# Optimization experiments

Hardware: AMD Instinct MI355X
Metric: run time of the kernel (lower is better)

## Reference

```python
import jax, jax.numpy as jnp
from jax import lax
import numpy as np

PATCH_H = 8
PATCH_W = 8


def setup_inputs() -> dict:
    key = jax.random.key(0)
    k1, k2 = jax.random.split(key)
    x = jax.random.normal(k1, (2, 1024, 256, 256), dtype=jnp.float32)
    # Conv1d weight [C_out, C_in, k], bias=False
    conv_w = jax.random.normal(k2, (1024, 1024, 3), dtype=jnp.float32) * 0.02
    return {"x": x, "conv_w": conv_w}


def reference(x, conv_w):
    B, C, H, W = x.shape
    hf, wf = H // PATCH_H, W // PATCH_W
    P = hf * wf
    # Patch average pool: mean over each (PATCH_H, PATCH_W) tile -> [B, C, hf, wf]
    xp = x.reshape(B, C, hf, PATCH_H, wf, PATCH_W)
    y = xp.mean(axis=(3, 5)).reshape(B, C, P)
    # Conv1d over the patch axis (SAME padding, no bias), then sigmoid gate
    g = lax.conv_general_dilated(
        y, conv_w, window_strides=(1,), padding="SAME",
        dimension_numbers=("NCH", "OIH", "NCH"))
    g = jax.nn.sigmoid(g).reshape(B, C, hf, wf)
    # Broadcast gate back over each patch and multiply
    out = xp * g[:, :, :, None, :, None]
    return out.reshape(B, C, H, W)
```

## Files before the change

kernel.cpp:

```cpp
#include <hip/hip_runtime.h>
#include <hip/hip_bf16.h>

#define HH 256
#define WW 256
#define CCH 1024
#define PP 1024

using f32x4 = __attribute__((ext_vector_type(4))) float;
using short8 = __attribute__((ext_vector_type(8))) short;

__global__ __launch_bounds__(256) void pool_kernel(const float* __restrict__ xb,
                                                   float* __restrict__ yb) {
    int c    = blockIdx.x;
    int wid  = threadIdx.x >> 6;
    int lane = threadIdx.x & 63;
    const float* xp = xb + (size_t)c * (HH * WW) + lane * 4;
    float* yp = yb + (size_t)c * PP;
#pragma unroll
    for (int s = 0; s < 8; ++s) {
        int ph = wid + s * 4;
        const float* slab = xp + (size_t)ph * 8 * WW;
        float acc = 0.f;
#pragma unroll
        for (int r = 0; r < 8; ++r) {
            f32x4 v = *(const f32x4*)(slab + (size_t)r * WW);
            acc += v.x + v.y + v.z + v.w;
        }
        acc += __shfl_xor(acc, 1);
        if ((lane & 1) == 0)
            yp[ph * 32 + (lane >> 1)] = acc * (1.f / 64.f);
    }
}

__global__ __launch_bounds__(256) void wconv_pad_kernel(const float* __restrict__ w,
                                                        __hip_bfloat16* __restrict__ wT,
                                                        __hip_bfloat16* __restrict__ yT) {
    int tid = blockIdx.x * 256 + threadIdx.x;
    const float* p = w + (size_t)tid * 3;
    wT[tid]               = __float2bfloat16(p[0]);
    wT[(1u << 20) + tid]  = __float2bfloat16(p[1]);
    wT[(2u << 20) + tid]  = __float2bfloat16(p[2]);
    if (tid < 2 * CCH) {
        int bb = tid >> 10, cc = tid & 1023;
        __hip_bfloat16 z = __float2bfloat16(0.f);
        __hip_bfloat16* base = yT + (size_t)bb * (PP + 2) * CCH;
        base[cc] = z;
        base[(size_t)(PP + 1) * CCH + cc] = z;
    }
}

__global__ __launch_bounds__(256) void transpose_kernel(const float* __restrict__ yb,
                                                        __hip_bfloat16* __restrict__ yTb) {
    int c0 = blockIdx.x * 32;
    int p0 = blockIdx.y * 32;
    __shared__ float tile[32][33];
    int tx = threadIdx.x, ty = threadIdx.y;
#pragma unroll
    for (int rr = 0; rr < 4; ++rr)
        tile[ty + rr * 8][tx] = yb[(size_t)(c0 + ty + rr * 8) * PP + p0 + tx];
    __syncthreads();
#pragma unroll
    for (int rr = 0; rr < 4; ++rr)
        yTb[(size_t)(1 + p0 + ty + rr * 8) * CCH + c0 + tx] =
            __float2bfloat16(tile[tx][ty + rr * 8]);
}

__global__ __launch_bounds__(512) void conv_gemm_kernel(
        const __hip_bfloat16* __restrict__ wT,
        const __hip_bfloat16* __restrict__ yTb,
        float* __restrict__ gateb) {
    int lane = threadIdx.x & 63;
    int wid  = threadIdx.x >> 6;
    int wp  = wid & 1, wco = wid >> 1;
    int l15 = lane & 15, lhi = lane >> 4;
    int co_base = blockIdx.x * 64 + wco * 16;
    int p_base  = blockIdx.y * 64 + wp * 32;
    f32x4 acc[2] = {};
#pragma unroll
    for (int tap = 0; tap < 3; ++tap) {
        const __hip_bfloat16* Ap = wT + (size_t)tap * (1u << 20)
                                 + (size_t)(co_base + l15) * CCH + lhi * 8;
        const __hip_bfloat16* Bp = yTb + (size_t)(p_base + l15 + tap) * CCH + lhi * 8;
        for (int ci0 = 0; ci0 < CCH; ci0 += 32) {
            short8 a0 = *(const short8*)(Ap + ci0);
            short8 b0 = *(const short8*)(Bp + ci0);
            short8 b1 = *(const short8*)(Bp + ci0 + 16 * CCH);
            acc[0] = __builtin_amdgcn_mfma_f32_16x16x32_bf16(a0, b0, acc[0], 0, 0, 0);
            acc[1] = __builtin_amdgcn_mfma_f32_16x16x32_bf16(a0, b1, acc[1], 0, 0, 0);
        }
    }
#pragma unroll
    for (int j16 = 0; j16 < 2; ++j16) {
        int col  = p_base + j16 * 16 + l15;
        int row0 = co_base + lhi * 4;
#pragma unroll
        for (int r = 0; r < 4; ++r)
            gateb[(size_t)(row0 + r) * PP + col] = 1.f / (1.f + __expf(-acc[j16][r]));
    }
}

__global__ __launch_bounds__(256) void apply_kernel(const float* __restrict__ xb,
                                                    const float* __restrict__ gateb,
                                                    float* __restrict__ outb) {
    int c = 1023 - blockIdx.x;
    const float* xp = xb   + (size_t)c * (HH * WW);
    float*       op = outb + (size_t)c * (HH * WW);
    __shared__ float g[PP];
    int t = threadIdx.x;
    ((f32x4*)g)[t] = ((const f32x4*)(gateb + (size_t)c * PP))[t];
    __syncthreads();
    int col4 = t & 63;
    int r    = t >> 6;
    int pc   = col4 >> 1;
#pragma unroll 4
    for (int it = 0; it < 64; ++it) {
        int row = it * 4 + r;
        float gg = g[(row >> 3) * 32 + pc];
        size_t off = (size_t)row * 64 + col4;
        f32x4 v = *((const f32x4*)xp + off);
        v *= gg;
        __builtin_nontemporal_store(v, (f32x4*)op + off);
    }
}

extern "C" void kernel_launch(void* const* d_in, const int* in_sizes, int n_in,
                              void* d_out, int out_size, void* d_ws, size_t ws_size,
                              hipStream_t stream) {
    const float* x = (const float*)d_in[0];
    const float* w = (const float*)d_in[1];
    float* out = (float*)d_out;

    char* ws = (char*)d_ws;
    float*          y    = (float*)(ws);
    __hip_bfloat16* yT   = (__hip_bfloat16*)(ws + 8388608);
    __hip_bfloat16* wT   = (__hip_bfloat16*)(ws + 12591104);
    float*          gate = (float*)(ws + 18882560);

    hipLaunchKernelGGL(wconv_pad_kernel, dim3(4096), dim3(256), 0, stream, w, wT, yT);
    for (int b = 0; b < 2; ++b) {
        const float* xb = x + (size_t)b * CCH * HH * WW;
        float* yb       = y + (size_t)b * CCH * PP;
        __hip_bfloat16* yTb = yT + (size_t)b * (PP + 2) * CCH;
        float* gateb    = gate + (size_t)b * CCH * PP;
        float* outb     = out + (size_t)b * CCH * HH * WW;
        hipLaunchKernelGGL(pool_kernel,      dim3(1024),      dim3(256),   0, stream, xb, yb);
        hipLaunchKernelGGL(transpose_kernel, dim3(32, 32),    dim3(32, 8), 0, stream, yb, yTb);
        hipLaunchKernelGGL(conv_gemm_kernel, dim3(16, 16),    dim3(512),   0, stream, wT, yTb, gateb);
        hipLaunchKernelGGL(apply_kernel,     dim3(1024),      dim3(256),   0, stream, xb, gateb, outb);
    }
}
```

Before: 412.8 us.

## Fuse pool with weight conversion and batch-0 apply with batch-1 pool

```diff
diff --git a/kernel.cpp b/kernel.cpp
--- a/kernel.cpp
+++ b/kernel.cpp
@@ -9,11 +9,10 @@
 using f32x4 = __attribute__((ext_vector_type(4))) float;
 using short8 = __attribute__((ext_vector_type(8))) short;
 
-__global__ __launch_bounds__(256) void pool_kernel(const float* __restrict__ xb,
-                                                   float* __restrict__ yb) {
-    int c    = blockIdx.x;
-    int wid  = threadIdx.x >> 6;
-    int lane = threadIdx.x & 63;
+__device__ __forceinline__ void pool_body(const float* __restrict__ xb,
+                                          float* __restrict__ yb, int c, int t) {
+    int wid  = t >> 6;
+    int lane = t & 63;
     const float* xp = xb + (size_t)c * (HH * WW) + lane * 4;
     float* yp = yb + (size_t)c * PP;
 #pragma unroll
@@ -32,21 +31,75 @@
     }
 }
 
-__global__ __launch_bounds__(256) void wconv_pad_kernel(const float* __restrict__ w,
-                                                        __hip_bfloat16* __restrict__ wT,
-                                                        __hip_bfloat16* __restrict__ yT) {
-    int tid = blockIdx.x * 256 + threadIdx.x;
-    const float* p = w + (size_t)tid * 3;
-    wT[tid]               = __float2bfloat16(p[0]);
-    wT[(1u << 20) + tid]  = __float2bfloat16(p[1]);
-    wT[(2u << 20) + tid]  = __float2bfloat16(p[2]);
-    if (tid < 2 * CCH) {
-        int bb = tid >> 10, cc = tid & 1023;
-        __hip_bfloat16 z = __float2bfloat16(0.f);
-        __hip_bfloat16* base = yT + (size_t)bb * (PP + 2) * CCH;
-        base[cc] = z;
-        base[(size_t)(PP + 1) * CCH + cc] = z;
+__device__ __forceinline__ void apply_body(const float* __restrict__ xb,
+                                           const float* __restrict__ gateb,
+                                           float* __restrict__ outb,
+                                           float* __restrict__ g,
+                                           int c, int t) {
+    const float* xp = xb   + (size_t)c * (HH * WW);
+    float*       op = outb + (size_t)c * (HH * WW);
+    ((f32x4*)g)[t] = ((const f32x4*)(gateb + (size_t)c * PP))[t];
+    __syncthreads();
+    int col4 = t & 63;
+    int r    = t >> 6;
+    int pc   = col4 >> 1;
+#pragma unroll 4
+    for (int it = 0; it < 64; ++it) {
+        int row = it * 4 + r;
+        float gg = g[(row >> 3) * 32 + pc];
+        size_t off = (size_t)row * 64 + col4;
+        f32x4 v = *((const f32x4*)xp + off);
+        v *= gg;
+        __builtin_nontemporal_store(v, (f32x4*)op + off);
     }
+}
+
+__global__ __launch_bounds__(256) void pool0_wconv_kernel(
+        const float* __restrict__ x, const float* __restrict__ w,
+        float* __restrict__ y, __hip_bfloat16* __restrict__ wT,
+        __hip_bfloat16* __restrict__ yT) {
+    int bid = blockIdx.x, t = threadIdx.x;
+    if (bid < 1024) {
+        pool_body(x, y, bid, t);
+    } else {
+        int base = (bid - 1024) * 256 + t;
+#pragma unroll
+        for (int it = 0; it < 16; ++it) {
+            int idx = it * (1 << 16) + base;
+            const float* p = w + (size_t)idx * 3;
+            wT[idx]               = __float2bfloat16(p[0]);
+            wT[(1u << 20) + idx]  = __float2bfloat16(p[1]);
+            wT[(2u << 20) + idx]  = __float2bfloat16(p[2]);
+        }
+        if (base < 2 * CCH) {
+            int bb = base >> 10, cc = base & 1023;
+            __hip_bfloat16 z = __float2bfloat16(0.f);
+            __hip_bfloat16* basep = yT + (size_t)bb * (PP + 2) * CCH;
+            basep[cc] = z;
+            basep[(size_t)(PP + 1) * CCH + cc] = z;
+        }
+    }
+}
+
+__global__ __launch_bounds__(256) void apply0_pool1_kernel(
+        const float* __restrict__ x, const float* __restrict__ gate,
+        float* __restrict__ out, float* __restrict__ y) {
+    __shared__ __align__(16) float g[PP];
+    int bid = blockIdx.x, t = threadIdx.x;
+    if (bid < 1024) {
+        apply_body(x, gate, out, g, 1023 - bid, t);
+    } else {
+        const float* x1 = x + (size_t)CCH * HH * WW;
+        float*       y1 = y + (size_t)CCH * PP;
+        pool_body(x1, y1, bid - 1024, t);
+    }
+}
+
+__global__ __launch_bounds__(256) void apply_kernel(const float* __restrict__ xb,
+                                                    const float* __restrict__ gateb,
+                                                    float* __restrict__ outb) {
+    __shared__ __align__(16) float g[PP];
+    apply_body(xb, gateb, outb, g, 1023 - blockIdx.x, threadIdx.x);
 }
 
 __global__ __launch_bounds__(256) void transpose_kernel(const float* __restrict__ yb,
@@ -65,16 +118,15 @@
             __float2bfloat16(tile[tx][ty + rr * 8]);
 }
 
-__global__ __launch_bounds__(512) void conv_gemm_kernel(
+__global__ __launch_bounds__(256) void conv_gemm_kernel(
         const __hip_bfloat16* __restrict__ wT,
         const __hip_bfloat16* __restrict__ yTb,
         float* __restrict__ gateb) {
     int lane = threadIdx.x & 63;
     int wid  = threadIdx.x >> 6;
-    int wp  = wid & 1, wco = wid >> 1;
     int l15 = lane & 15, lhi = lane >> 4;
-    int co_base = blockIdx.x * 64 + wco * 16;
-    int p_base  = blockIdx.y * 64 + wp * 32;
+    int co_base = blockIdx.x * 64 + wid * 16;
+    int p_base  = blockIdx.y * 32;
     f32x4 acc[2] = {};
 #pragma unroll
     for (int tap = 0; tap < 3; ++tap) {
@@ -99,30 +151,6 @@
     }
 }
 
-__global__ __launch_bounds__(256) void apply_kernel(const float* __restrict__ xb,
-                                                    const float* __restrict__ gateb,
-                                                    float* __restrict__ outb) {
-    int c = 1023 - blockIdx.x;
-    const float* xp = xb   + (size_t)c * (HH * WW);
-    float*       op = outb + (size_t)c * (HH * WW);
-    __shared__ float g[PP];
-    int t = threadIdx.x;
-    ((f32x4*)g)[t] = ((const f32x4*)(gateb + (size_t)c * PP))[t];
-    __syncthreads();
-    int col4 = t & 63;
-    int r    = t >> 6;
-    int pc   = col4 >> 1;
-#pragma unroll 4
-    for (int it = 0; it < 64; ++it) {
-        int row = it * 4 + r;
-        float gg = g[(row >> 3) * 32 + pc];
-        size_t off = (size_t)row * 64 + col4;
-        f32x4 v = *((const f32x4*)xp + off);
-        v *= gg;
-        __builtin_nontemporal_store(v, (f32x4*)op + off);
-    }
-}
-
 extern "C" void kernel_launch(void* const* d_in, const int* in_sizes, int n_in,
                               void* d_out, int out_size, void* d_ws, size_t ws_size,
                               hipStream_t stream) {
@@ -136,16 +164,19 @@
     __hip_bfloat16* wT   = (__hip_bfloat16*)(ws + 12591104);
     float*          gate = (float*)(ws + 18882560);
 
-    hipLaunchKernelGGL(wconv_pad_kernel, dim3(4096), dim3(256), 0, stream, w, wT, yT);
-    for (int b = 0; b < 2; ++b) {
-        const float* xb = x + (size_t)b * CCH * HH * WW;
-        float* yb       = y + (size_t)b * CCH * PP;
-        __hip_bfloat16* yTb = yT + (size_t)b * (PP + 2) * CCH;
-        float* gateb    = gate + (size_t)b * CCH * PP;
-        float* outb     = out + (size_t)b * CCH * HH * WW;
-        hipLaunchKernelGGL(pool_kernel,      dim3(1024),      dim3(256),   0, stream, xb, yb);
-        hipLaunchKernelGGL(transpose_kernel, dim3(32, 32),    dim3(32, 8), 0, stream, yb, yTb);
-        hipLaunchKernelGGL(conv_gemm_kernel, dim3(16, 16),    dim3(512),   0, stream, wT, yTb, gateb);
-        hipLaunchKernelGGL(apply_kernel,     dim3(1024),      dim3(256),   0, stream, xb, gateb, outb);
-    }
+    const float* x1    = x    + (size_t)CCH * HH * WW;
+    float*       y1    = y    + (size_t)CCH * PP;
+    __hip_bfloat16* yT1 = yT  + (size_t)(PP + 2) * CCH;
+    float*       gate1 = gate + (size_t)CCH * PP;
+    float*       out1  = out  + (size_t)CCH * HH * WW;
+
+    hipLaunchKernelGGL(pool0_wconv_kernel, dim3(1280), dim3(256), 0, stream,
+                       x, w, y, wT, yT);
+    hipLaunchKernelGGL(transpose_kernel, dim3(32, 32), dim3(32, 8), 0, stream, y, yT);
+    hipLaunchKernelGGL(conv_gemm_kernel, dim3(16, 32), dim3(256), 0, stream, wT, yT, gate);
+    hipLaunchKernelGGL(apply0_pool1_kernel, dim3(2048), dim3(256), 0, stream,
+                       x, gate, out, y);
+    hipLaunchKernelGGL(transpose_kernel, dim3(32, 32), dim3(32, 8), 0, stream, y1, yT1);
+    hipLaunchKernelGGL(conv_gemm_kernel, dim3(16, 32), dim3(256), 0, stream, wT, yT1, gate1);
+    hipLaunchKernelGGL(apply_kernel, dim3(1024), dim3(256), 0, stream, x1, gate1, out1);
 }
```

Measured after the change: 414.7 us. Within noise of the previous version (+0.5%).
